# Optimization experiments

Hardware: AMD Instinct MI355X
Metric: run time of the kernel (lower is better)

Reference implementation:

```python
import jax, jax.numpy as jnp
import numpy as np

B, T, C = 8, 1024, 1024
H, D = 16, 64  # num_heads, head_size

def setup_inputs() -> dict:
    key = jax.random.key(0)
    ks = jax.random.split(key, 6)
    s = C ** -0.5
    return {
        "x": jax.random.normal(ks[0], (B, T, C), dtype=jnp.float32),
        "Wq": jax.random.normal(ks[1], (H, C, D), dtype=jnp.float32) * s,
        "Wk": jax.random.normal(ks[2], (H, C, D), dtype=jnp.float32) * s,
        "Wv": jax.random.normal(ks[3], (H, C, D), dtype=jnp.float32) * s,
        "Wproj": jax.random.normal(ks[4], (H * D, C), dtype=jnp.float32) * ((H * D) ** -0.5),
        "bproj": jnp.zeros((C,), dtype=jnp.float32),
    }

def reference(x, Wq, Wk, Wv, Wproj, bproj):
    # per-head QKV projections, batched over heads via einsum (same math as looped heads)
    q = jnp.einsum('btc,hcd->bhtd', x, Wq)
    k = jnp.einsum('btc,hcd->bhtd', x, Wk)
    v = jnp.einsum('btc,hcd->bhtd', x, Wv)
    scale = D ** -0.5  # k.shape[-1]**-0.5 in original head
    scores = jnp.einsum('bhtd,bhsd->bhts', q, k) * scale  # [B,H,T,T]
    Tn = x.shape[1]
    causal = jnp.tril(jnp.ones((Tn, Tn), dtype=bool))
    scores = jnp.where(causal, scores, jnp.float32(-jnp.inf))
    att = jax.nn.softmax(scores, axis=-1)
    out = jnp.einsum('bhts,bhsd->bhtd', att, v)          # [B,H,T,D]
    out = out.transpose(0, 2, 1, 3).reshape(x.shape[0], Tn, H * D)  # concat heads
    return out @ Wproj + bproj  # dropout is identity at p=0.0
```

## Files before the change

### kernel.cpp

```cpp
#include <hip/hip_runtime.h>
#include <hip/hip_bf16.h>

#define B_ 8
#define T_ 1024
#define C_ 1024
#define H_ 16
#define D_ 64
#define QKVLD 3072

typedef short v8s __attribute__((ext_vector_type(8)));
typedef float v4f __attribute__((ext_vector_type(4)));
typedef float v16f __attribute__((ext_vector_type(16)));

__device__ __forceinline__ unsigned short f2b(float f) {
    unsigned int u = __builtin_bit_cast(unsigned int, f);
    unsigned int lsb = (u >> 16) & 1u;
    u += 0x7fffu + lsb;
    return (unsigned short)(u >> 16);
}

__device__ __forceinline__ float fexp2(float x) {
#if __has_builtin(__builtin_amdgcn_exp2f)
    return __builtin_amdgcn_exp2f(x);
#else
    return __expf(x * 0.69314718056f);
#endif
}

#define GLOAD16(gp, lp)                                                          \
    __builtin_amdgcn_global_load_lds(                                            \
        (const __attribute__((address_space(1))) unsigned int*)(gp),             \
        (__attribute__((address_space(3))) unsigned int*)(lp), 16, 0, 0)

__global__ void cast_x_kernel(const float* __restrict__ x, unsigned short* __restrict__ y, int n) {
    int i = (blockIdx.x * 256 + threadIdx.x) * 4;
    if (i < n) {
        float4 v = *(const float4*)(x + i);
        ushort4 o;
        o.x = f2b(v.x); o.y = f2b(v.y); o.z = f2b(v.z); o.w = f2b(v.w);
        *(ushort4*)(y + i) = o;
    }
}

__global__ void transpose_wqkv(const float* __restrict__ Wq, const float* __restrict__ Wk,
                               const float* __restrict__ Wv, unsigned short* __restrict__ WqkvT) {
    int z = blockIdx.y;
    int h = z / 3, part = z % 3;
    const float* src = (part == 0 ? Wq : (part == 1 ? Wk : Wv)) + (size_t)h * C_ * D_;
    int c0 = blockIdx.x * 64;
    __shared__ unsigned short t[64][65];
    for (int i = threadIdx.x; i < 4096; i += 256) {
        int r = i >> 6, d = i & 63;
        t[d][r] = f2b(src[(size_t)(c0 + r) * D_ + d]);
    }
    __syncthreads();
    unsigned short* dst = WqkvT + (size_t)(h * 192 + part * 64) * C_;
    for (int i = threadIdx.x; i < 4096; i += 256) {
        int d = i >> 6, r = i & 63;
        dst[(size_t)d * C_ + c0 + r] = t[d][r];
    }
}

__global__ void transpose_wproj(const float* __restrict__ W, unsigned short* __restrict__ Wt) {
    int k0 = blockIdx.y * 64, n0 = blockIdx.x * 64;
    __shared__ unsigned short t[64][65];
    for (int i = threadIdx.x; i < 4096; i += 256) {
        int r = i >> 6, c = i & 63;
        t[c][r] = f2b(W[(size_t)(k0 + r) * C_ + n0 + c]);
    }
    __syncthreads();
    for (int i = threadIdx.x; i < 4096; i += 256) {
        int n = i >> 6, k = i & 63;
        Wt[(size_t)(n0 + n) * 1024 + k0 + k] = t[n][k];
    }
}

__global__ __launch_bounds__(256, 2) void gemm_qkv(const unsigned short* __restrict__ A,
                                                   const unsigned short* __restrict__ Bt,
                                                   unsigned short* __restrict__ Cout,
                                                   int M, int N, int K) {
    __shared__ unsigned short lA[2][256 * 32];
    __shared__ unsigned short lB[2][128 * 32];
    int tid = threadIdx.x;
    int m0 = blockIdx.y * 256, n0 = blockIdx.x * 128;
    int lane = tid & 63, w = tid >> 6;
    int half = lane >> 5, l32 = lane & 31;
    int wm = w >> 1, wn = w & 1;

    const unsigned short* gA[4];
    int offA[4];
    #pragma unroll
    for (int j = 0; j < 4; j++) {
        int c = j * 256 + tid;
        int row = c >> 2;
        int col8 = ((c & 3) ^ ((row >> 1) & 3)) * 8;
        gA[j] = A + (size_t)(m0 + row) * K + col8;
        offA[j] = (j * 256 + w * 64) * 16;
    }
    const unsigned short* gB[2];
    int offB[2];
    #pragma unroll
    for (int j = 0; j < 2; j++) {
        int c = j * 256 + tid;
        int row = c >> 2;
        int col8 = ((c & 3) ^ ((row >> 1) & 3)) * 8;
        gB[j] = Bt + (size_t)(n0 + row) * K + col8;
        offB[j] = (j * 256 + w * 64) * 16;
    }

    int am[4], bn[2];
    #pragma unroll
    for (int mi = 0; mi < 4; mi++) am[mi] = wm * 128 + mi * 32 + l32;
    #pragma unroll
    for (int ni = 0; ni < 2; ni++) bn[ni] = wn * 64 + ni * 32 + l32;

    v16f acc[4][2];
    #pragma unroll
    for (int mi = 0; mi < 4; mi++)
        #pragma unroll
        for (int ni = 0; ni < 2; ni++)
            #pragma unroll
            for (int r = 0; r < 16; r++) acc[mi][ni][r] = 0.f;

    int ktiles = K >> 5;
    #pragma unroll
    for (int j = 0; j < 4; j++) GLOAD16(gA[j], (char*)&lA[0][0] + offA[j]);
    #pragma unroll
    for (int j = 0; j < 2; j++) GLOAD16(gB[j], (char*)&lB[0][0] + offB[j]);

    for (int it = 0; it < ktiles; it++) {
        int cur = it & 1, nxt = cur ^ 1;
        __asm__ volatile("s_waitcnt vmcnt(0)" ::: "memory");
        __asm__ volatile("s_barrier" ::: "memory");
        {
            int kn = (it + 1 < ktiles) ? (it + 1) * 32 : it * 32;
            #pragma unroll
            for (int j = 0; j < 4; j++) GLOAD16(gA[j] + kn, (char*)&lA[nxt][0] + offA[j]);
            #pragma unroll
            for (int j = 0; j < 2; j++) GLOAD16(gB[j] + kn, (char*)&lB[nxt][0] + offB[j]);
        }
        #pragma unroll
        for (int step = 0; step < 2; step++) {
            int g = step * 2 + half;
            v8s af[4], bf[2];
            #pragma unroll
            for (int mi = 0; mi < 4; mi++)
                af[mi] = *(const v8s*)&lA[cur][am[mi] * 32 + ((g ^ ((am[mi] >> 1) & 3)) * 8)];
            #pragma unroll
            for (int ni = 0; ni < 2; ni++)
                bf[ni] = *(const v8s*)&lB[cur][bn[ni] * 32 + ((g ^ ((bn[ni] >> 1) & 3)) * 8)];
            #pragma unroll
            for (int mi = 0; mi < 4; mi++)
                #pragma unroll
                for (int ni = 0; ni < 2; ni++)
                    acc[mi][ni] = __builtin_amdgcn_mfma_f32_32x32x16_bf16(af[mi], bf[ni], acc[mi][ni], 0, 0, 0);
        }
    }
    #pragma unroll
    for (int mi = 0; mi < 4; mi++) {
        #pragma unroll
        for (int ni = 0; ni < 2; ni++) {
            int col = n0 + wn * 64 + ni * 32 + l32;
            #pragma unroll
            for (int r = 0; r < 16; r++) {
                int row = m0 + wm * 128 + mi * 32 + (r & 3) + 8 * (r >> 2) + 4 * half;
                Cout[(size_t)row * N + col] = f2b(acc[mi][ni][r]);
            }
        }
    }
}

__global__ __launch_bounds__(256, 3) void gemm_proj(const unsigned short* __restrict__ A,
                                                    const unsigned short* __restrict__ Bt,
                                                    float* __restrict__ Cout,
                                                    const float* __restrict__ bias,
                                                    int M, int N, int K) {
    constexpr int ABUF = 128 * 32;
    constexpr int BBUF = 128 * 32;
    __shared__ unsigned short lA[3 * ABUF];
    __shared__ unsigned short lB[3 * BBUF];

    int tid = threadIdx.x;
    int lane = tid & 63, w = tid >> 6;
    int half = lane >> 5, l32 = lane & 31;
    int wm = w >> 1, wn = w & 1;

    int g = blockIdx.x;
    int nbm = M / 128;
    int stripe = nbm >> 3;
    int xcd = g & 7, s = g >> 3;
    int m0 = (xcd * stripe + (s % stripe)) * 128;
    int n0 = (s / stripe) * 128;

    const unsigned short* gA[2];
    int offA[2];
    #pragma unroll
    for (int j = 0; j < 2; j++) {
        int c = j * 256 + tid;
        int row = c >> 2;
        int col8 = ((c & 3) ^ ((row >> 1) & 3)) * 8;
        gA[j] = A + (size_t)(m0 + row) * K + col8;
        offA[j] = (j * 256 + w * 64) * 16;
    }
    const unsigned short* gB[2];
    int offB[2];
    #pragma unroll
    for (int j = 0; j < 2; j++) {
        int c = j * 256 + tid;
        int row = c >> 2;
        int col8 = ((c & 3) ^ ((row >> 1) & 3)) * 8;
        gB[j] = Bt + (size_t)(n0 + row) * K + col8;
        offB[j] = (j * 256 + w * 64) * 16;
    }

    int am[2], bn[2];
    #pragma unroll
    for (int mi = 0; mi < 2; mi++) am[mi] = wm * 64 + mi * 32 + l32;
    #pragma unroll
    for (int ni = 0; ni < 2; ni++) bn[ni] = wn * 64 + ni * 32 + l32;

    v16f acc[2][2];
    #pragma unroll
    for (int mi = 0; mi < 2; mi++)
        #pragma unroll
        for (int ni = 0; ni < 2; ni++)
            #pragma unroll
            for (int r = 0; r < 16; r++) acc[mi][ni][r] = 0.f;

    int kt = K >> 5;
    #pragma unroll
    for (int j = 0; j < 2; j++) GLOAD16(gA[j], (char*)lA + offA[j]);
    #pragma unroll
    for (int j = 0; j < 2; j++) GLOAD16(gB[j], (char*)lB + offB[j]);
    #pragma unroll
    for (int j = 0; j < 2; j++) GLOAD16(gA[j] + 32, (char*)(lA + ABUF) + offA[j]);
    #pragma unroll
    for (int j = 0; j < 2; j++) GLOAD16(gB[j] + 32, (char*)(lB + BBUF) + offB[j]);

    int cur = 0;
    for (int it = 0; it < kt; it++) {
        int nx2 = cur + 2; if (nx2 >= 3) nx2 -= 3;
        __asm__ volatile("s_waitcnt vmcnt(4)" ::: "memory");
        __asm__ volatile("s_barrier" ::: "memory");
        {
            int kn = ((it + 2 < kt) ? it + 2 : kt - 1) << 5;
            #pragma unroll
            for (int j = 0; j < 2; j++) GLOAD16(gA[j] + kn, (char*)(lA + nx2 * ABUF) + offA[j]);
            #pragma unroll
            for (int j = 0; j < 2; j++) GLOAD16(gB[j] + kn, (char*)(lB + nx2 * BBUF) + offB[j]);
        }
        const unsigned short* bufA = lA + cur * ABUF;
        const unsigned short* bufB = lB + cur * BBUF;
        #pragma unroll
        for (int step = 0; step < 2; step++) {
            int gch = step * 2 + half;
            v8s af[2], bf[2];
            #pragma unroll
            for (int mi = 0; mi < 2; mi++)
                af[mi] = *(const v8s*)&bufA[am[mi] * 32 + ((gch ^ ((am[mi] >> 1) & 3)) * 8)];
            #pragma unroll
            for (int ni = 0; ni < 2; ni++)
                bf[ni] = *(const v8s*)&bufB[bn[ni] * 32 + ((gch ^ ((bn[ni] >> 1) & 3)) * 8)];
            #pragma unroll
            for (int mi = 0; mi < 2; mi++)
                #pragma unroll
                for (int ni = 0; ni < 2; ni++)
                    acc[mi][ni] = __builtin_amdgcn_mfma_f32_32x32x16_bf16(af[mi], bf[ni], acc[mi][ni], 0, 0, 0);
        }
        cur = cur + 1; if (cur >= 3) cur -= 3;
    }
    #pragma unroll
    for (int mi = 0; mi < 2; mi++) {
        #pragma unroll
        for (int ni = 0; ni < 2; ni++) {
            int col = n0 + wn * 64 + ni * 32 + l32;
            #pragma unroll
            for (int r = 0; r < 16; r++) {
                int row = m0 + wm * 64 + mi * 32 + (r & 3) + 8 * (r >> 2) + 4 * half;
                Cout[(size_t)row * N + col] = acc[mi][ni][r] + bias[col];
            }
        }
    }
}

__global__ void transpose_v(const unsigned short* __restrict__ QKV, unsigned short* __restrict__ Vt) {
    int t0 = blockIdx.x * 64;
    int bh = blockIdx.y;
    int b = bh >> 4, h = bh & 15;
    __shared__ unsigned short t[64][65];
    for (int i = threadIdx.x; i < 4096; i += 256) {
        int r = i >> 6, d = i & 63;
        t[d][r] = QKV[(size_t)(b * T_ + t0 + r) * QKVLD + h * 192 + 128 + d];
    }
    __syncthreads();
    for (int i = threadIdx.x; i < 4096; i += 256) {
        int d = i >> 6, r = i & 63;
        Vt[((size_t)bh * 64 + d) * T_ + t0 + r] = t[d][r];
    }
}

__global__ __launch_bounds__(256) void attn_kernel(const unsigned short* __restrict__ QKV,
                                                   const unsigned short* __restrict__ Vt,
                                                   unsigned short* __restrict__ Ob) {
    int bh = blockIdx.x;
    int qt = 7 - blockIdx.y;
    int b = bh >> 4, h = bh & 15;
    int tid = threadIdx.x, lane = tid & 63, w = tid >> 6;
    int quad = lane >> 4, l16 = lane & 15;
    int qg0 = qt * 128 + w * 32;

    __shared__ unsigned short lK[2][2][64][32];
    __shared__ unsigned short lV[2][64][32];
    __shared__ unsigned short lP[4][32][76];

    v8s aq[2][2];
    #pragma unroll
    for (int st = 0; st < 2; st++) {
        const unsigned short* qp = QKV + (size_t)(b * T_ + qg0 + st * 16 + l16) * QKVLD + h * 192;
        aq[st][0] = *(const v8s*)(qp + quad * 8);
        aq[st][1] = *(const v8s*)(qp + 32 + quad * 8);
    }

    const unsigned short* gK[2];
    const unsigned short* gV[2];
    int ldsOff[2];
    #pragma unroll
    for (int j = 0; j < 2; j++) {
        int c = j * 256 + tid;
        int halfp = c >> 8, row = (c >> 2) & 63;
        int col8 = ((c & 3) ^ ((row >> 1) & 3)) * 8;
        gK[j] = QKV + (size_t)(b * T_ + row) * QKVLD + h * 192 + 64 + halfp * 32 + col8;
        gV[j] = Vt + ((size_t)bh * 64 + row) * T_ + halfp * 32 + col8;
        ldsOff[j] = (j * 256 + w * 64) * 16;
    }
    int rcol = (quad ^ ((l16 >> 1) & 3)) * 8;

    v4f accO[2][4];
    float lsum[2][4];
    #pragma unroll
    for (int st = 0; st < 2; st++)
        #pragma unroll
        for (int i = 0; i < 4; i++) { accO[st][i] = (v4f){0.f, 0.f, 0.f, 0.f}; lsum[st][i] = 0.f; }

    int ntiles = 2 * qt + 2;
    const float SC = 0.1803368801f;

    #pragma unroll
    for (int j = 0; j < 2; j++)
        GLOAD16(gK[j], (char*)&lK[0][0][0][0] + ldsOff[j]);

    for (int it = 0; it < ntiles; it++) {
        int cur = it & 1, nxt = cur ^ 1;
        int s0 = it * 64;
        __asm__ volatile("s_waitcnt vmcnt(0)" ::: "memory");
        __asm__ volatile("s_barrier" ::: "memory");
        #pragma unroll
        for (int j = 0; j < 2; j++)
            GLOAD16(gV[j] + s0, (char*)&lV[0][0][0] + ldsOff[j]);
        __asm__ volatile("" ::: "memory");
        {
            int itn = (it + 1 < ntiles) ? it + 1 : it;
            size_t koff = (size_t)itn * 64 * QKVLD;
            #pragma unroll
            for (int j = 0; j < 2; j++)
                GLOAD16(gK[j] + koff, (char*)&lK[nxt][0][0][0] + ldsOff[j]);
        }
        bool act0 = (qg0 + 15 >= s0);
        bool act1 = (qg0 + 31 >= s0);
        if (act1) {
            v4f sf[2][4];
            #pragma unroll
            for (int nt = 0; nt < 4; nt++) {
                v8s bk0 = *(const v8s*)&lK[cur][0][nt * 16 + l16][rcol];
                v8s bk1 = *(const v8s*)&lK[cur][1][nt * 16 + l16][rcol];
                if (act0) {
                    v4f a = (v4f){0.f, 0.f, 0.f, 0.f};
                    a = __builtin_amdgcn_mfma_f32_16x16x32_bf16(aq[0][0], bk0, a, 0, 0, 0);
                    a = __builtin_amdgcn_mfma_f32_16x16x32_bf16(aq[0][1], bk1, a, 0, 0, 0);
                    sf[0][nt] = a;
                }
                v4f a1 = (v4f){0.f, 0.f, 0.f, 0.f};
                a1 = __builtin_amdgcn_mfma_f32_16x16x32_bf16(aq[1][0], bk0, a1, 0, 0, 0);
                a1 = __builtin_amdgcn_mfma_f32_16x16x32_bf16(aq[1][1], bk1, a1, 0, 0, 0);
                sf[1][nt] = a1;
            }
            bool diag = (it >= ntiles - 2);
            #pragma unroll
            for (int st = 0; st < 2; st++) {
                if (st == 0 && !act0) continue;
                if (diag) {
                    #pragma unroll
                    for (int nt = 0; nt < 4; nt++)
                        #pragma unroll
                        for (int r = 0; r < 4; r++) {
                            int sg = s0 + nt * 16 + l16;
                            int qg = qg0 + st * 16 + quad * 4 + r;
                            float p = (sg > qg) ? 0.f : fexp2(sf[st][nt][r] * SC);
                            lsum[st][r] += p;
                            lP[w][st * 16 + quad * 4 + r][nt * 16 + l16] = f2b(p);
                        }
                } else {
                    #pragma unroll
                    for (int nt = 0; nt < 4; nt++)
                        #pragma unroll
                        for (int r = 0; r < 4; r++) {
                            float p = fexp2(sf[st][nt][r] * SC);
                            lsum[st][r] += p;
                            lP[w][st * 16 + quad * 4 + r][nt * 16 + l16] = f2b(p);
                        }
                }
            }
        }
        __asm__ volatile("s_waitcnt vmcnt(2)" ::: "memory");
        __asm__ volatile("s_barrier" ::: "memory");
        __asm__ volatile("s_waitcnt lgkmcnt(0)" ::: "memory");
        if (act1) {
            #pragma unroll
            for (int sc = 0; sc < 2; sc++) {
                v8s ap0, ap1;
                if (act0) ap0 = *(const v8s*)&lP[w][l16][sc * 32 + quad * 8];
                ap1 = *(const v8s*)&lP[w][16 + l16][sc * 32 + quad * 8];
                #pragma unroll
                for (int dt = 0; dt < 4; dt++) {
                    v8s bv = *(const v8s*)&lV[sc][dt * 16 + l16][rcol];
                    if (act0) accO[0][dt] = __builtin_amdgcn_mfma_f32_16x16x32_bf16(ap0, bv, accO[0][dt], 0, 0, 0);
                    accO[1][dt] = __builtin_amdgcn_mfma_f32_16x16x32_bf16(ap1, bv, accO[1][dt], 0, 0, 0);
                }
            }
        }
    }
    #pragma unroll
    for (int st = 0; st < 2; st++)
        #pragma unroll
        for (int r = 0; r < 4; r++) {
            float s = lsum[st][r];
            #pragma unroll
            for (int off = 1; off < 16; off <<= 1) s += __shfl_xor(s, off, 64);
            float inv = 1.0f / s;
            int q = qg0 + st * 16 + quad * 4 + r;
            #pragma unroll
            for (int dt = 0; dt < 4; dt++) {
                int d = dt * 16 + l16;
                Ob[(size_t)(b * T_ + q) * (H_ * D_) + h * 64 + d] = f2b(accO[st][dt][r] * inv);
            }
        }
}

extern "C" void kernel_launch(void* const* d_in, const int* in_sizes, int n_in,
                              void* d_out, int out_size, void* d_ws, size_t ws_size,
                              hipStream_t stream) {
    const float* x     = (const float*)d_in[0];
    const float* Wq    = (const float*)d_in[1];
    const float* Wk    = (const float*)d_in[2];
    const float* Wv    = (const float*)d_in[3];
    const float* Wproj = (const float*)d_in[4];
    const float* bproj = (const float*)d_in[5];
    float* out = (float*)d_out;

    char* ws = (char*)d_ws;
    unsigned short* xb     = (unsigned short*)ws;
    unsigned short* WqkvT  = (unsigned short*)(ws + 16777216);
    unsigned short* WprojT = (unsigned short*)(ws + 23068672);
    unsigned short* QKV    = (unsigned short*)(ws + 25165824);
    unsigned short* Vt     = (unsigned short*)(ws + 75497472);
    unsigned short* Ob     = (unsigned short*)(ws + 92274688);

    cast_x_kernel<<<dim3(8192), dim3(256), 0, stream>>>(x, xb, B_ * T_ * C_);
    transpose_wqkv<<<dim3(16, 48), dim3(256), 0, stream>>>(Wq, Wk, Wv, WqkvT);
    transpose_wproj<<<dim3(16, 16), dim3(256), 0, stream>>>(Wproj, WprojT);
    gemm_qkv<<<dim3(24, 32), dim3(256), 0, stream>>>(xb, WqkvT, QKV, 8192, 3072, 1024);
    transpose_v<<<dim3(16, 128), dim3(256), 0, stream>>>(QKV, Vt);
    attn_kernel<<<dim3(128, 8), dim3(256), 0, stream>>>(QKV, Vt, Ob);
    gemm_proj<<<dim3(512), dim3(256), 0, stream>>>(Ob, WprojT, out, bproj, 8192, 1024, 1024);
}
```

Baseline: 241.9 us.

## Keep attention probabilities in registers and merge prep kernels into one launch

The QK^T MFMA operands are swapped so the score fragments come out transposed. The exponentiated probabilities can then be packed straight into bf16 registers and fed to 16x16x16 MFMAs for the PV product, with no round trip through the lP shared-memory buffer. This removes LDS writes and reads and the per-row shuffle reduction, but it uses twice as many smaller MFMAs, round-half-up bf16 packing, and __expf in place of exp2. The x cast and the two weight transposes are also merged into a single launch to cut launch overhead.

```diff
diff --git a/kernel.cpp b/kernel.cpp
--- a/kernel.cpp
+++ b/kernel.cpp
@@ -8,6 +8,7 @@
 #define D_ 64
 #define QKVLD 3072
 
+typedef short v4s __attribute__((ext_vector_type(4)));
 typedef short v8s __attribute__((ext_vector_type(8)));
 typedef float v4f __attribute__((ext_vector_type(4)));
 typedef float v16f __attribute__((ext_vector_type(16)));
@@ -20,58 +21,69 @@
 }
 
 __device__ __forceinline__ float fexp2(float x) {
-#if __has_builtin(__builtin_amdgcn_exp2f)
-    return __builtin_amdgcn_exp2f(x);
-#else
     return __expf(x * 0.69314718056f);
-#endif
-}
+}
+
+__device__ __forceinline__ v4s pack4(float p0, float p1, float p2, float p3) {
+    unsigned int a = (__builtin_bit_cast(unsigned int, p0) + 0x8000u) >> 16;
+    unsigned int b = (__builtin_bit_cast(unsigned int, p1) + 0x8000u) & 0xFFFF0000u;
+    unsigned int c = (__builtin_bit_cast(unsigned int, p2) + 0x8000u) >> 16;
+    unsigned int d = (__builtin_bit_cast(unsigned int, p3) + 0x8000u) & 0xFFFF0000u;
+    union { unsigned int u[2]; v4s v; } t;
+    t.u[0] = a | b; t.u[1] = c | d;
+    return t.v;
+}
+
+#define MFMA32(A, B, C) __builtin_amdgcn_mfma_f32_16x16x32_bf16(A, B, C, 0, 0, 0)
+#define MFMA16(A, B, C) __builtin_amdgcn_mfma_f32_16x16x16bf16_1k(A, B, C, 0, 0, 0)
 
 #define GLOAD16(gp, lp)                                                          \
     __builtin_amdgcn_global_load_lds(                                            \
         (const __attribute__((address_space(1))) unsigned int*)(gp),             \
         (__attribute__((address_space(3))) unsigned int*)(lp), 16, 0, 0)
 
-__global__ void cast_x_kernel(const float* __restrict__ x, unsigned short* __restrict__ y, int n) {
-    int i = (blockIdx.x * 256 + threadIdx.x) * 4;
-    if (i < n) {
+__global__ void prep_kernel(const float* __restrict__ x, const float* __restrict__ Wq,
+                            const float* __restrict__ Wk, const float* __restrict__ Wv,
+                            const float* __restrict__ Wproj,
+                            unsigned short* __restrict__ xb,
+                            unsigned short* __restrict__ WqkvT,
+                            unsigned short* __restrict__ WprojT) {
+    __shared__ unsigned short t[64][65];
+    int g = blockIdx.x;
+    if (g < 8192) {
+        int i = (g * 256 + (int)threadIdx.x) * 4;
         float4 v = *(const float4*)(x + i);
         ushort4 o;
         o.x = f2b(v.x); o.y = f2b(v.y); o.z = f2b(v.z); o.w = f2b(v.w);
-        *(ushort4*)(y + i) = o;
-    }
-}
-
-__global__ void transpose_wqkv(const float* __restrict__ Wq, const float* __restrict__ Wk,
-                               const float* __restrict__ Wv, unsigned short* __restrict__ WqkvT) {
-    int z = blockIdx.y;
-    int h = z / 3, part = z % 3;
-    const float* src = (part == 0 ? Wq : (part == 1 ? Wk : Wv)) + (size_t)h * C_ * D_;
-    int c0 = blockIdx.x * 64;
-    __shared__ unsigned short t[64][65];
-    for (int i = threadIdx.x; i < 4096; i += 256) {
-        int r = i >> 6, d = i & 63;
-        t[d][r] = f2b(src[(size_t)(c0 + r) * D_ + d]);
-    }
-    __syncthreads();
-    unsigned short* dst = WqkvT + (size_t)(h * 192 + part * 64) * C_;
-    for (int i = threadIdx.x; i < 4096; i += 256) {
-        int d = i >> 6, r = i & 63;
-        dst[(size_t)d * C_ + c0 + r] = t[d][r];
-    }
-}
-
-__global__ void transpose_wproj(const float* __restrict__ W, unsigned short* __restrict__ Wt) {
-    int k0 = blockIdx.y * 64, n0 = blockIdx.x * 64;
-    __shared__ unsigned short t[64][65];
-    for (int i = threadIdx.x; i < 4096; i += 256) {
-        int r = i >> 6, c = i & 63;
-        t[c][r] = f2b(W[(size_t)(k0 + r) * C_ + n0 + c]);
-    }
-    __syncthreads();
-    for (int i = threadIdx.x; i < 4096; i += 256) {
-        int n = i >> 6, k = i & 63;
-        Wt[(size_t)(n0 + n) * 1024 + k0 + k] = t[n][k];
+        *(ushort4*)(xb + i) = o;
+    } else if (g < 8192 + 768) {
+        int idx = g - 8192;
+        int z = idx >> 4;
+        int h = z / 3, part = z % 3;
+        const float* src = (part == 0 ? Wq : (part == 1 ? Wk : Wv)) + (size_t)h * C_ * D_;
+        int c0 = (idx & 15) * 64;
+        for (int i = threadIdx.x; i < 4096; i += 256) {
+            int r = i >> 6, d = i & 63;
+            t[d][r] = f2b(src[(size_t)(c0 + r) * D_ + d]);
+        }
+        __syncthreads();
+        unsigned short* dst = WqkvT + (size_t)(h * 192 + part * 64) * C_;
+        for (int i = threadIdx.x; i < 4096; i += 256) {
+            int d = i >> 6, r = i & 63;
+            dst[(size_t)d * C_ + c0 + r] = t[d][r];
+        }
+    } else {
+        int idx = g - 8960;
+        int n0 = (idx & 15) * 64, k0 = (idx >> 4) * 64;
+        for (int i = threadIdx.x; i < 4096; i += 256) {
+            int r = i >> 6, c = i & 63;
+            t[c][r] = f2b(Wproj[(size_t)(k0 + r) * C_ + n0 + c]);
+        }
+        __syncthreads();
+        for (int i = threadIdx.x; i < 4096; i += 256) {
+            int n = i >> 6, k = i & 63;
+            WprojT[(size_t)(n0 + n) * 1024 + k0 + k] = t[n][k];
+        }
     }
 }
 
@@ -311,7 +323,6 @@
 
     __shared__ unsigned short lK[2][2][64][32];
     __shared__ unsigned short lV[2][64][32];
-    __shared__ unsigned short lP[4][32][76];
 
     v8s aq[2][2];
     #pragma unroll
@@ -336,11 +347,11 @@
     int rcol = (quad ^ ((l16 >> 1) & 3)) * 8;
 
     v4f accO[2][4];
-    float lsum[2][4];
+    float lsum[2] = {0.f, 0.f};
     #pragma unroll
     for (int st = 0; st < 2; st++)
         #pragma unroll
-        for (int i = 0; i < 4; i++) { accO[st][i] = (v4f){0.f, 0.f, 0.f, 0.f}; lsum[st][i] = 0.f; }
+        for (int i = 0; i < 4; i++) accO[st][i] = (v4f){0.f, 0.f, 0.f, 0.f};
 
     int ntiles = 2 * qt + 2;
     const float SC = 0.1803368801f;
@@ -367,76 +378,73 @@
         }
         bool act0 = (qg0 + 15 >= s0);
         bool act1 = (qg0 + 31 >= s0);
+        v4s pP[2][4];
         if (act1) {
             v4f sf[2][4];
             #pragma unroll
             for (int nt = 0; nt < 4; nt++) {
                 v8s bk0 = *(const v8s*)&lK[cur][0][nt * 16 + l16][rcol];
                 v8s bk1 = *(const v8s*)&lK[cur][1][nt * 16 + l16][rcol];
+                v4f a1 = (v4f){0.f, 0.f, 0.f, 0.f};
+                a1 = MFMA32(bk0, aq[1][0], a1);
+                a1 = MFMA32(bk1, aq[1][1], a1);
+                sf[1][nt] = a1;
                 if (act0) {
-                    v4f a = (v4f){0.f, 0.f, 0.f, 0.f};
-                    a = __builtin_amdgcn_mfma_f32_16x16x32_bf16(aq[0][0], bk0, a, 0, 0, 0);
-                    a = __builtin_amdgcn_mfma_f32_16x16x32_bf16(aq[0][1], bk1, a, 0, 0, 0);
-                    sf[0][nt] = a;
+                    v4f a0 = (v4f){0.f, 0.f, 0.f, 0.f};
+                    a0 = MFMA32(bk0, aq[0][0], a0);
+                    a0 = MFMA32(bk1, aq[0][1], a0);
+                    sf[0][nt] = a0;
                 }
-                v4f a1 = (v4f){0.f, 0.f, 0.f, 0.f};
-                a1 = __builtin_amdgcn_mfma_f32_16x16x32_bf16(aq[1][0], bk0, a1, 0, 0, 0);
-                a1 = __builtin_amdgcn_mfma_f32_16x16x32_bf16(aq[1][1], bk1, a1, 0, 0, 0);
-                sf[1][nt] = a1;
             }
             bool diag = (it >= ntiles - 2);
             #pragma unroll
             for (int st = 0; st < 2; st++) {
                 if (st == 0 && !act0) continue;
-                if (diag) {
+                int qg = qg0 + st * 16 + l16;
+                #pragma unroll
+                for (int nt = 0; nt < 4; nt++) {
+                    float p[4];
                     #pragma unroll
-                    for (int nt = 0; nt < 4; nt++)
-                        #pragma unroll
-                        for (int r = 0; r < 4; r++) {
-                            int sg = s0 + nt * 16 + l16;
-                            int qg = qg0 + st * 16 + quad * 4 + r;
-                            float p = (sg > qg) ? 0.f : fexp2(sf[st][nt][r] * SC);
-                            lsum[st][r] += p;
-                            lP[w][st * 16 + quad * 4 + r][nt * 16 + l16] = f2b(p);
+                    for (int r = 0; r < 4; r++) {
+                        if (diag) {
+                            int sg = s0 + nt * 16 + quad * 4 + r;
+                            p[r] = (sg > qg) ? 0.f : fexp2(sf[st][nt][r] * SC);
+                        } else {
+                            p[r] = fexp2(sf[st][nt][r] * SC);
                         }
-                } else {
-                    #pragma unroll
-                    for (int nt = 0; nt < 4; nt++)
-                        #pragma unroll
-                        for (int r = 0; r < 4; r++) {
-                            float p = fexp2(sf[st][nt][r] * SC);
-                            lsum[st][r] += p;
-                            lP[w][st * 16 + quad * 4 + r][nt * 16 + l16] = f2b(p);
-                        }
+                        lsum[st] += p[r];
+                    }
+                    pP[st][nt] = pack4(p[0], p[1], p[2], p[3]);
                 }
             }
         }
         __asm__ volatile("s_waitcnt vmcnt(2)" ::: "memory");
         __asm__ volatile("s_barrier" ::: "memory");
-        __asm__ volatile("s_waitcnt lgkmcnt(0)" ::: "memory");
         if (act1) {
             #pragma unroll
-            for (int sc = 0; sc < 2; sc++) {
-                v8s ap0, ap1;
-                if (act0) ap0 = *(const v8s*)&lP[w][l16][sc * 32 + quad * 8];
-                ap1 = *(const v8s*)&lP[w][16 + l16][sc * 32 + quad * 8];
+            for (int kb = 0; kb < 4; kb++) {
+                int sc_ = kb >> 1;
+                int ccg = (kb & 1) * 2 + (quad >> 1);
                 #pragma unroll
                 for (int dt = 0; dt < 4; dt++) {
-                    v8s bv = *(const v8s*)&lV[sc][dt * 16 + l16][rcol];
-                    if (act0) accO[0][dt] = __builtin_amdgcn_mfma_f32_16x16x32_bf16(ap0, bv, accO[0][dt], 0, 0, 0);
-                    accO[1][dt] = __builtin_amdgcn_mfma_f32_16x16x32_bf16(ap1, bv, accO[1][dt], 0, 0, 0);
+                    int d = dt * 16 + l16;
+                    int ccp = ccg ^ ((l16 >> 1) & 3);
+                    v4s bv = *(const v4s*)&lV[sc_][d][ccp * 8 + (quad & 1) * 4];
+                    accO[1][dt] = MFMA16(pP[1][kb], bv, accO[1][dt]);
+                    if (act0) accO[0][dt] = MFMA16(pP[0][kb], bv, accO[0][dt]);
                 }
             }
         }
     }
     #pragma unroll
-    for (int st = 0; st < 2; st++)
+    for (int st = 0; st < 2; st++) {
+        float ls = lsum[st];
+        ls += __shfl_xor(ls, 16, 64);
+        ls += __shfl_xor(ls, 32, 64);
         #pragma unroll
         for (int r = 0; r < 4; r++) {
-            float s = lsum[st][r];
-            #pragma unroll
-            for (int off = 1; off < 16; off <<= 1) s += __shfl_xor(s, off, 64);
-            float inv = 1.0f / s;
+            float lq = __shfl(ls, quad * 4 + r, 64);
+            float inv = 1.0f / lq;
             int q = qg0 + st * 16 + quad * 4 + r;
             #pragma unroll
             for (int dt = 0; dt < 4; dt++) {
@@ -444,6 +452,7 @@
                 Ob[(size_t)(b * T_ + q) * (H_ * D_) + h * 64 + d] = f2b(accO[st][dt][r] * inv);
             }
         }
+    }
 }
 
 extern "C" void kernel_launch(void* const* d_in, const int* in_sizes, int n_in,
@@ -465,9 +474,7 @@
     unsigned short* Vt     = (unsigned short*)(ws + 75497472);
     unsigned short* Ob     = (unsigned short*)(ws + 92274688);
 
-    cast_x_kernel<<<dim3(8192), dim3(256), 0, stream>>>(x, xb, B_ * T_ * C_);
-    transpose_wqkv<<<dim3(16, 48), dim3(256), 0, stream>>>(Wq, Wk, Wv, WqkvT);
-    transpose_wproj<<<dim3(16, 16), dim3(256), 0, stream>>>(Wproj, WprojT);
+    prep_kernel<<<dim3(9216), dim3(256), 0, stream>>>(x, Wq, Wk, Wv, Wproj, xb, WqkvT, WprojT);
     gemm_qkv<<<dim3(24, 32), dim3(256), 0, stream>>>(xb, WqkvT, QKV, 8192, 3072, 1024);
     transpose_v<<<dim3(16, 128), dim3(256), 0, stream>>>(QKV, Vt);
     attn_kernel<<<dim3(128, 8), dim3(256), 0, stream>>>(QKV, Vt, Ob);
```

Measured after the change: 240.7 us. Within noise of the previous version (-0.5%).
